# Performance work log

Measured on AMD Instinct MI355X. Metric: run time of the kernel, lower is better.

The kernel has to match this reference:

```python
import jax, jax.numpy as jnp
import numpy as np

SCALE = 1.0 / np.sqrt(64.0).astype(np.float32)  # module hardcodes 64**0.5

def setup_inputs() -> dict:
    key = jax.random.key(0)
    kx, kw = jax.random.split(key)
    B, S, D, O = 8, 2048, 768, 768
    x = jax.random.normal(kx, (B, S, D), dtype=jnp.float32)
    # keras 'uniform' initializer: U(-0.05, 0.05)
    kernel = jax.random.uniform(kw, (3, D, O), dtype=jnp.float32, minval=-0.05, maxval=0.05)
    return {"x": x, "kernel": kernel}

def reference(x, kernel):
    # x: [B,S,D], kernel: [3,D,O]
    WQ = jnp.einsum('bsd,do->bso', x, kernel[0])
    WK = jnp.einsum('bsd,do->bso', x, kernel[1])
    WV = jnp.einsum('bsd,do->bso', x, kernel[2])
    QK = jnp.einsum('bso,bto->bst', WQ, WK) * SCALE  # [B,S,S]
    A = jax.nn.softmax(QK, axis=-1)
    return jnp.einsum('bst,bto->bso', A, WV)
```

## Files before the change

### kernel.cpp

```cpp
#include <hip/hip_runtime.h>


typedef _Float16 f16;
typedef _Float16 f16x8 __attribute__((ext_vector_type(8)));
typedef _Float16 f16x4 __attribute__((ext_vector_type(4)));
typedef float f32x4 __attribute__((ext_vector_type(4)));

__device__ __forceinline__ void gload16(const void* g, void* l) {
    __builtin_amdgcn_global_load_lds((__attribute__((address_space(1))) void*)g,
                                     (__attribute__((address_space(3))) void*)l,
                                     16, 0, 0);
}

template <int MODE, typename OutT>
__global__ __launch_bounds__(256, 2)
void gemm_bt(const f16* __restrict__ A, const f16* __restrict__ B,
             OutT* __restrict__ C, float* R, int K, int lda, int ldb, int ldc,
             long sA, long sB, long sC, float oscale)
{
    __shared__ __align__(16) f16 lA[128 * 64];
    __shared__ __align__(16) f16 lB[128 * 64];

    const int tid  = threadIdx.x;
    const int wave = tid >> 6;
    const int lane = tid & 63;

    const unsigned gx = gridDim.x, gy = gridDim.y;
    const unsigned nb = gx * gy * gridDim.z;
    unsigned lin = blockIdx.x + gx * (blockIdx.y + gy * blockIdx.z);
    if ((nb & 7u) == 0u) lin = (lin & 7u) * (nb >> 3) + (lin >> 3);
    const unsigned bx = lin % gx;
    const unsigned rem = lin / gx;
    const unsigned by = rem % gy;
    const unsigned bz = rem / gy;

    A += (long)bz * sA;
    B += (long)bz * sB;
    C += (long)bz * sC;

    const long row0 = (long)by * 128;
    const long col0 = (long)bx * 128;

    const int r0 = tid >> 3;
    const int cs = (((tid & 7) ^ (r0 & 7)) * 8);
    const f16* ag0 = A + (row0 +      r0) * lda + cs;
    const f16* ag1 = A + (row0 + 32 + r0) * lda + cs;
    const f16* ag2 = A + (row0 + 64 + r0) * lda + cs;
    const f16* ag3 = A + (row0 + 96 + r0) * lda + cs;
    const f16* bg0 = B + (col0 +      r0) * ldb + cs;
    const f16* bg1 = B + (col0 + 32 + r0) * ldb + cs;
    const f16* bg2 = B + (col0 + 64 + r0) * ldb + cs;
    const f16* bg3 = B + (col0 + 96 + r0) * ldb + cs;
    f16* lA0 = lA +        wave * 512;
    f16* lA1 = lA + 2048 + wave * 512;
    f16* lA2 = lA + 4096 + wave * 512;
    f16* lA3 = lA + 6144 + wave * 512;
    f16* lB0 = lB +        wave * 512;
    f16* lB1 = lB + 2048 + wave * 512;
    f16* lB2 = lB + 4096 + wave * 512;
    f16* lB3 = lB + 6144 + wave * 512;

    const int wm = wave >> 1, wn = wave & 1;
    const int fl = lane & 15;
    const int q  = lane >> 4;
    const int co = ((q ^ (fl & 7)) * 8);
    const f16* paw = lA + (wm * 64 + fl) * 64;
    const f16* pbw = lB + (wn * 64 + fl) * 64;

    f32x4 acc[4][4] = {};

    for (int k0 = 0; k0 < K; k0 += 64) {
        __syncthreads();
        gload16(ag0, lA0); gload16(ag1, lA1);
        gload16(ag2, lA2); gload16(ag3, lA3);
        gload16(bg0, lB0); gload16(bg1, lB1);
        gload16(bg2, lB2); gload16(bg3, lB3);
        ag0 += 64; ag1 += 64; ag2 += 64; ag3 += 64;
        bg0 += 64; bg1 += 64; bg2 += 64; bg3 += 64;
        __syncthreads();

#pragma unroll
        for (int kk = 0; kk < 64; kk += 32) {
            const int o = co ^ (kk == 0 ? 0 : 32);
            f16x8 a[4], b[4];
#pragma unroll
            for (int i = 0; i < 4; ++i)
                a[i] = *(const f16x8*)(paw + i * 1024 + o);
#pragma unroll
            for (int j = 0; j < 4; ++j)
                b[j] = *(const f16x8*)(pbw + j * 1024 + o);
#pragma unroll
            for (int i = 0; i < 4; ++i)
#pragma unroll
                for (int j = 0; j < 4; ++j)
                    acc[i][j] = __builtin_amdgcn_mfma_f32_16x16x32_f16(
                        a[i], b[j], acc[i][j], 0, 0, 0);
        }
    }

    const int rq = (lane >> 4) * 4;
    if (MODE != 0) R += (long)bz * 2048;
#pragma unroll
    for (int i = 0; i < 4; ++i) {
#pragma unroll
        for (int r = 0; r < 4; ++r) {
            const long row = row0 + wm * 64 + i * 16 + rq + r;
            if (MODE == 0) {
#pragma unroll
                for (int j = 0; j < 4; ++j) {
                    const long col = col0 + wn * 64 + j * 16 + fl;
                    C[row * ldc + col] = (OutT)(acc[i][j][r] * oscale);
                }
            } else if (MODE == 1) {
                float s = 0.f;
#pragma unroll
                for (int j = 0; j < 4; ++j) {
                    const long col = col0 + wn * 64 + j * 16 + fl;
                    float e = __expf(acc[i][j][r] - 12.0f);
                    C[row * ldc + col] = (OutT)e;
                    s += e;
                }
                s += __shfl_xor(s, 1, 16);
                s += __shfl_xor(s, 2, 16);
                s += __shfl_xor(s, 4, 16);
                s += __shfl_xor(s, 8, 16);
                if (fl == 0) atomicAdd(&R[row], s);
            } else {
                const float inv = 1.0f / R[row];
#pragma unroll
                for (int j = 0; j < 4; ++j) {
                    const long col = col0 + wn * 64 + j * 16 + fl;
                    C[row * ldc + col] = (OutT)(acc[i][j][r] * inv);
                }
            }
        }
    }
}

__global__ void cvt_f32_f16(const float* __restrict__ in, f16* __restrict__ out,
                            int n4)
{
    int i = blockIdx.x * blockDim.x + threadIdx.x;
    int stride = gridDim.x * blockDim.x;
    for (; i < n4; i += stride) {
        float4 v = ((const float4*)in)[i];
        f16x4 h;
        h[0] = (f16)v.x; h[1] = (f16)v.y; h[2] = (f16)v.z; h[3] = (f16)v.w;
        ((f16x4*)out)[i] = h;
    }
}

__global__ void wtrans(const float* __restrict__ w, f16* __restrict__ wT)
{
    __shared__ float t[32][33];
    const int o0 = blockIdx.x * 32, d0 = blockIdx.y * 32;
    const int tx = threadIdx.x & 31, ty = threadIdx.x >> 5;
    const float* src = w + (size_t)d0 * 768 + o0;
#pragma unroll
    for (int r = 0; r < 32; r += 8)
        t[ty + r][tx] = src[(size_t)(ty + r) * 768 + tx];
    __syncthreads();
    f16* dst = wT + (size_t)o0 * 768 + d0;
#pragma unroll
    for (int r = 0; r < 32; r += 8)
        dst[(size_t)(ty + r) * 768 + tx] = (f16)t[tx][ty + r];
}

extern "C" void kernel_launch(void* const* d_in, const int* in_sizes, int n_in,
                              void* d_out, int out_size, void* d_ws, size_t ws_size,
                              hipStream_t stream)
{
    (void)in_sizes; (void)n_in; (void)out_size; (void)ws_size;
    const float* x = (const float*)d_in[0];
    const float* w = (const float*)d_in[1];
    float* out = (float*)d_out;

    const long NX = 12582912;
    const long NW = 1769472;
    const long NW1 = 589824;
    f16* xh  = (f16*)d_ws;
    f16* wh  = xh + NX;
    f16* wt2 = wh + NW;
    f16* GT  = wt2 + NW1;
    f16* XG  = GT + NW1;
    f16* Vt  = XG + NX;
    f16* Sc  = Vt + NX;
    float* R = (float*)wh;

    cvt_f32_f16<<<2048, 256, 0, stream>>>(x, xh, (int)(NX / 4));
    cvt_f32_f16<<<1024, 256, 0, stream>>>(w, wh, (int)(NW / 4));
    wtrans<<<dim3(24, 24, 1), 256, 0, stream>>>(w + 2 * NW1, wt2);

    gemm_bt<0, f16><<<dim3(6, 6, 1), 256, 0, stream>>>(
        wh + NW1, wh, GT, nullptr, 768, 768, 768, 768, 0, 0, 0, 0.125f);
    gemm_bt<0, f16><<<dim3(6, 128, 1), 256, 0, stream>>>(
        xh, GT, XG, nullptr, 768, 768, 768, 768, 0, 0, 0, 1.0f);
    gemm_bt<0, f16><<<dim3(16, 6, 8), 256, 0, stream>>>(
        wt2, xh, Vt, nullptr, 768, 768, 768, 2048, 0, 1572864, 1572864, 1.0f);
    hipMemsetAsync(R, 0, 8 * 2048 * sizeof(float), stream);
    gemm_bt<1, f16><<<dim3(16, 16, 8), 256, 0, stream>>>(
        XG, xh, Sc, R, 768, 768, 768, 2048, 1572864, 1572864, 4194304, 1.0f);
    gemm_bt<2, float><<<dim3(6, 16, 8), 256, 0, stream>>>(
        Sc, Vt, out, R, 2048, 2048, 2048, 768, 4194304, 1572864, 1572864, 1.0f);
}
```

Measured before the change: 297.0 us.

## Merge XG and V projection GEMMs into one launch, raise occupancy hint

The two independent projection GEMMs (x·G and Wv^T·x^T) now run in a single kernel whose grid splits blocks between the two problems, so there is one launch and a larger combined grid. The GEMM body is factored into a device function, and the launch bounds go from 2 to 5 blocks per CU for all GEMMs. The higher occupancy hint may force register spills or reduce unrolling in the 4x4 MFMA accumulator loop.

```diff
diff --git a/kernel.cpp b/kernel.cpp
--- a/kernel.cpp
+++ b/kernel.cpp
@@ -13,10 +13,10 @@
 }
 
 template <int MODE, typename OutT>
-__global__ __launch_bounds__(256, 2)
-void gemm_bt(const f16* __restrict__ A, const f16* __restrict__ B,
-             OutT* __restrict__ C, float* R, int K, int lda, int ldb, int ldc,
-             long sA, long sB, long sC, float oscale)
+__device__ __forceinline__ void gemm_core(
+    const f16* __restrict__ A, const f16* __restrict__ B,
+    OutT* __restrict__ C, float* __restrict__ R,
+    int K, int lda, int ldb, int ldc, long row0, long col0, float oscale)
 {
     __shared__ __align__(16) f16 lA[128 * 64];
     __shared__ __align__(16) f16 lB[128 * 64];
@@ -24,22 +24,6 @@
     const int tid  = threadIdx.x;
     const int wave = tid >> 6;
     const int lane = tid & 63;
-
-    const unsigned gx = gridDim.x, gy = gridDim.y;
-    const unsigned nb = gx * gy * gridDim.z;
-    unsigned lin = blockIdx.x + gx * (blockIdx.y + gy * blockIdx.z);
-    if ((nb & 7u) == 0u) lin = (lin & 7u) * (nb >> 3) + (lin >> 3);
-    const unsigned bx = lin % gx;
-    const unsigned rem = lin / gx;
-    const unsigned by = rem % gy;
-    const unsigned bz = rem / gy;
-
-    A += (long)bz * sA;
-    B += (long)bz * sB;
-    C += (long)bz * sC;
-
-    const long row0 = (long)by * 128;
-    const long col0 = (long)bx * 128;
 
     const int r0 = tid >> 3;
     const int cs = (((tid & 7) ^ (r0 & 7)) * 8);
@@ -99,7 +83,6 @@
     }
 
     const int rq = (lane >> 4) * 4;
-    if (MODE != 0) R += (long)bz * 2048;
 #pragma unroll
     for (int i = 0; i < 4; ++i) {
 #pragma unroll
@@ -137,6 +120,66 @@
     }
 }
 
+template <int MODE, typename OutT>
+__global__ __launch_bounds__(256, 5)
+void gemm_bt(const f16* __restrict__ A, const f16* __restrict__ B,
+             OutT* __restrict__ C, float* R, int K, int lda, int ldb, int ldc,
+             long sA, long sB, long sC, float oscale)
+{
+    const unsigned gx = gridDim.x, gy = gridDim.y;
+    const unsigned nb = gx * gy * gridDim.z;
+    unsigned lin = blockIdx.x + gx * (blockIdx.y + gy * blockIdx.z);
+    if ((nb & 7u) == 0u) lin = (lin & 7u) * (nb >> 3) + (lin >> 3);
+    const unsigned bx = lin % gx;
+    const unsigned rem = lin / gx;
+    const unsigned by = rem % gy;
+    const unsigned bz = rem / gy;
+
+    gemm_core<MODE, OutT>(A + (long)bz * sA, B + (long)bz * sB,
+                          C + (long)bz * sC,
+                          (MODE != 0) ? (R + (long)bz * 2048) : nullptr,
+                          K, lda, ldb, ldc,
+                          (long)by * 128, (long)bx * 128, oscale);
+}
+
+__global__ __launch_bounds__(256, 5)
+void proj_dual(const f16* __restrict__ xh, const f16* __restrict__ GT,
+               f16* __restrict__ XG, const f16* __restrict__ wt2,
+               f16* __restrict__ Vt)
+{
+    const unsigned nb = 16u * 6u * 16u;
+    unsigned lin = blockIdx.x + 16u * (blockIdx.y + 6u * blockIdx.z);
+    lin = (lin & 7u) * (nb >> 3) + (lin >> 3);
+    const unsigned bx = lin % 16u;
+    const unsigned rem = lin / 16u;
+    const unsigned by = rem % 6u;
+    const unsigned bz = rem / 6u;
+
+    const f16 *Aa, *Bb;
+    f16* Cc;
+    int ldc_;
+    long r0_, c0_;
+    if (bz < 8u) {
+        Aa = wt2;
+        Bb = xh + (long)bz * 1572864;
+        Cc = Vt + (long)bz * 1572864;
+        ldc_ = 2048;
+        r0_ = (long)by * 128;
+        c0_ = (long)bx * 128;
+    } else {
+        const unsigned l = bx + 16u * by;
+        const unsigned xbx = l % 6u;
+        const unsigned xby = (bz - 8u) * 16u + l / 6u;
+        Aa = xh;
+        Bb = GT;
+        Cc = XG;
+        ldc_ = 768;
+        r0_ = (long)xby * 128;
+        c0_ = (long)xbx * 128;
+    }
+    gemm_core<0, f16>(Aa, Bb, Cc, nullptr, 768, 768, 768, ldc_, r0_, c0_, 1.0f);
+}
+
 __global__ void cvt_f32_f16(const float* __restrict__ in, f16* __restrict__ out,
                             int n4)
 {
@@ -175,8 +218,8 @@
     const float* w = (const float*)d_in[1];
     float* out = (float*)d_out;
 
-    const long NX = 12582912;
-    const long NW = 1769472;
+    const long NX  = 12582912;
+    const long NW  = 1769472;
     const long NW1 = 589824;
     f16* xh  = (f16*)d_ws;
     f16* wh  = xh + NX;
@@ -193,10 +236,7 @@
 
     gemm_bt<0, f16><<<dim3(6, 6, 1), 256, 0, stream>>>(
         wh + NW1, wh, GT, nullptr, 768, 768, 768, 768, 0, 0, 0, 0.125f);
-    gemm_bt<0, f16><<<dim3(6, 128, 1), 256, 0, stream>>>(
-        xh, GT, XG, nullptr, 768, 768, 768, 768, 0, 0, 0, 1.0f);
-    gemm_bt<0, f16><<<dim3(16, 6, 8), 256, 0, stream>>>(
-        wt2, xh, Vt, nullptr, 768, 768, 768, 2048, 0, 1572864, 1572864, 1.0f);
+    proj_dual<<<dim3(16, 6, 16), 256, 0, stream>>>(xh, GT, XG, wt2, Vt);
     hipMemsetAsync(R, 0, 8 * 2048 * sizeof(float), stream);
     gemm_bt<1, f16><<<dim3(16, 16, 8), 256, 0, stream>>>(
         XG, xh, Sc, R, 768, 768, 768, 2048, 1572864, 1572864, 4194304, 1.0f);
```

New measurement: 583.0 us. +96.3%, slower.
